# Kernel optimization log

Measured on AMD Instinct MI355X. Metric: run time of the kernel, lower is better.

Reference implementation:

```python
import jax, jax.numpy as jnp
import numpy as np

EMBED_DIM = 2048
NUM_HEADS = 16
HEAD_DIM = EMBED_DIM // NUM_HEADS  # 128
GROUP = 256
NEG = -1e9


def setup_inputs() -> dict:
    key = jax.random.key(0)
    ks = jax.random.split(key, 4)
    B, N, C = 2, 8192, EMBED_DIM
    s = 1.0 / np.sqrt(C).astype(np.float32)
    return {
        "x": jax.random.normal(ks[0], (B, N, C), jnp.float32),
        "Wq": jax.random.normal(ks[1], (C, C), jnp.float32) * s,
        "bq": jnp.zeros((C,), jnp.float32),
        "Wk": jax.random.normal(ks[2], (C, C), jnp.float32) * s,
        "bk": jnp.zeros((C,), jnp.float32),
        "Wv": jax.random.normal(ks[3], (C, C), jnp.float32) * s,
        "bv": jnp.zeros((C,), jnp.float32),
    }


def _s2_attn(x, Wq, bq, Wk, bk, Wv, bv):
    B, N, C = x.shape
    H, hd, gs = NUM_HEADS, HEAD_DIM, GROUP
    G = N // gs
    half = H // 2

    def heads(t):  # [B,N,C] -> [B,H,N,hd]
        return t.reshape(B, N, H, hd).transpose(0, 2, 1, 3)

    q = heads(x @ Wq.T + bq)
    k = heads(x @ Wk.T + bk)
    v = heads(x @ Wv.T + bv)

    def shift(t, s):  # shift second half of heads along sequence
        return jnp.concatenate([t[:, :half], jnp.roll(t[:, half:], s, axis=2)], axis=1)

    q, k, v = shift(q, -(gs // 2)), shift(k, -(gs // 2)), shift(v, -(gs // 2))

    # group-local attention: [B,H,G,gs,hd]
    qg = q.reshape(B, H, G, gs, hd)
    kg = k.reshape(B, H, G, gs, hd)
    vg = v.reshape(B, H, G, gs, hd)

    scores = jnp.einsum("bhgqd,bhgkd->bhgqk", qg, kg) / np.sqrt(hd).astype(x.dtype)
    causal = jnp.triu(jnp.ones((gs, gs), bool), 1)  # mask strictly-upper triangle
    scores = jnp.where(causal, NEG, scores)
    attn = jax.nn.softmax(scores, axis=-1)
    out = jnp.einsum("bhgqk,bhgkd->bhgqd", attn, vg).reshape(B, H, N, hd)

    out = shift(out, gs // 2)  # un-shift the shifted heads
    return out.transpose(0, 2, 1, 3).reshape(B, N, C)


def reference(x, Wq, bq, Wk, bk, Wv, bv):
    return _s2_attn(x, Wq, bq, Wk, bk, Wv, bv)
```

## Files before the change

### kernel.cpp

```cpp
#include <hip/hip_runtime.h>
#include <hip/hip_bf16.h>

#define NSEQ 8192
#define CDIM 2048
#define NHEAD 16
#define HD 128

typedef short short8 __attribute__((ext_vector_type(8)));
typedef short short4v __attribute__((ext_vector_type(4)));
typedef float float4v __attribute__((ext_vector_type(4)));

__device__ __forceinline__ short f2bf(float f) {
    __hip_bfloat16 h = __float2bfloat16(f);
    return *reinterpret_cast<short*>(&h);
}

__device__ __forceinline__ void async_load16(const short* g, short* l) {
    __builtin_amdgcn_global_load_lds((const __attribute__((address_space(1))) void*)g,
                                     (__attribute__((address_space(3))) void*)l,
                                     16, 0, 0);
}

#define X8 (33554432 / 8)
#define W8 (4194304 / 8)

__global__ __launch_bounds__(256) void cvt_all(
    const float* __restrict__ x, const float* __restrict__ wq,
    const float* __restrict__ wk, const float* __restrict__ wv,
    short* __restrict__ xb, short* __restrict__ wqb,
    short* __restrict__ wkb, short* __restrict__ wvb)
{
    const size_t i = (size_t)blockIdx.x * blockDim.x + threadIdx.x;
    const float* src;
    short* dst;
    size_t off;
    if (i < X8)              { src = x;  dst = xb;  off = i; }
    else if (i < X8 + W8)    { src = wq; dst = wqb; off = i - X8; }
    else if (i < X8 + 2*W8)  { src = wk; dst = wkb; off = i - X8 - W8; }
    else                     { src = wv; dst = wvb; off = i - X8 - 2*(size_t)W8; }
    const float4v a = ((const float4v*)src)[off * 2];
    const float4v b = ((const float4v*)src)[off * 2 + 1];
    short8 o;
    for (int j = 0; j < 4; j++) { o[j] = f2bf(a[j]); o[4 + j] = f2bf(b[j]); }
    ((short8*)dst)[off] = o;
}

__global__ __launch_bounds__(256, 2) void qkv_gemm(
    const short* __restrict__ x,
    const short* __restrict__ Wq, const float* __restrict__ bq,
    const short* __restrict__ Wk, const float* __restrict__ bk,
    const short* __restrict__ Wv, const float* __restrict__ bv,
    float* __restrict__ qout, short* __restrict__ kt, short* __restrict__ vt)
{
    __shared__ short As[128 * 32];
    __shared__ short Bs[128 * 32];

    const int tid  = threadIdx.x;
    const int wave = tid >> 6;
    const int lane = tid & 63;
    const int quad = lane >> 4;
    const int l15  = lane & 15;
    const int wm   = wave >> 1;
    const int wn   = wave & 1;

    const int m0  = blockIdx.x * 128;
    const int mat = blockIdx.y >> 4;
    const int h   = blockIdx.y & 15;
    const int n0  = h * HD;

    const short* W    = (mat == 0) ? Wq : (mat == 1) ? Wk : Wv;
    const float* bias = (mat == 0) ? bq : (mat == 1) ? bk : bv;

    const int srow = lane >> 2;
    const int scol = (lane & 3) * 8;

    const float4v fzero = {0.f, 0.f, 0.f, 0.f};
    float4v acc[4][4];
    for (int i = 0; i < 4; i++)
        for (int j = 0; j < 4; j++)
            acc[i][j] = fzero;

    for (int k0 = 0; k0 < CDIM; k0 += 32) {
        __syncthreads();
        for (int c = 0; c < 2; c++) {
            const int chunk = wave * 2 + c;
            const int row   = chunk * 16 + srow;
            async_load16(x + (size_t)(m0 + row) * CDIM + k0 + scol, &As[chunk * 512]);
            async_load16(W + (size_t)(n0 + row) * CDIM + k0 + scol, &Bs[chunk * 512]);
        }
        __syncthreads();

        short8 af[4], bf[4];
        for (int i = 0; i < 4; i++)
            af[i] = *(const short8*)&As[(wm * 64 + i * 16 + l15) * 32 + quad * 8];
        for (int j = 0; j < 4; j++)
            bf[j] = *(const short8*)&Bs[(wn * 64 + j * 16 + l15) * 32 + quad * 8];
        for (int i = 0; i < 4; i++)
            for (int j = 0; j < 4; j++)
                acc[i][j] = __builtin_amdgcn_mfma_f32_16x16x32_bf16(af[i], bf[j],
                                                                    acc[i][j], 0, 0, 0);
    }

    float bvals[4];
    for (int j = 0; j < 4; j++)
        bvals[j] = bias[n0 + wn * 64 + j * 16 + l15];

    for (int i = 0; i < 4; i++) {
        for (int j = 0; j < 4; j++) {
            const int d = wn * 64 + j * 16 + l15;
            for (int r = 0; r < 4; r++) {
                const int m   = m0 + wm * 64 + i * 16 + quad * 4 + r;
                const int b   = m >> 13;
                const int seq = m & (NSEQ - 1);
                const float v = acc[i][j][r] + bvals[j];
                if (mat == 0) {
                    qout[((size_t)(b * NSEQ + seq) << 11) + n0 + d] = v;
                } else {
                    short* outp = (mat == 1) ? kt : vt;
                    outp[(((size_t)(b * NHEAD + h) * NSEQ + seq) << 7) + d] = f2bf(v);
                }
            }
        }
    }
}

__global__ __launch_bounds__(512, 2) void s2_attn(const float* qsrc,
                                                  const short* __restrict__ kt,
                                                  const short* __restrict__ vt,
                                                  float* out)
{
    __shared__ short Ks[64 * 136];
    __shared__ short Vs[64 * 132];
    __shared__ short Ps[8][32 * 40];

    const int bx = blockIdx.x;
    const int g  = bx & 31;
    const int h  = (bx >> 5) & 15;
    const int b  = bx >> 9;
    const int shift = (h >= 8) ? 128 : 0;
    const int sbase = g * 256 + shift;

    const int tid  = threadIdx.x;
    const int wave = tid >> 6;
    const int lane = tid & 63;
    const int quad = lane >> 4;
    const int l15  = lane & 15;

    const size_t bh = ((size_t)b * NHEAD + h) * NSEQ;
    const short* kg = kt + bh * HD;
    const short* vg = vt + bh * HD;

    const int mt0 = wave * 2;

    short8 qf[2][4];
    for (int im = 0; im < 2; im++) {
        const int row = (mt0 + im) * 16 + l15;
        const int p   = (sbase + row) & (NSEQ - 1);
        const float* qr = qsrc + (((size_t)(b * NSEQ + p)) << 11) + h * HD;
        for (int ks = 0; ks < 4; ks++) {
            const float4v qa = *(const float4v*)(qr + ks * 32 + quad * 8);
            const float4v qb = *(const float4v*)(qr + ks * 32 + quad * 8 + 4);
            short8 f;
            for (int j = 0; j < 4; j++) { f[j] = f2bf(qa[j]); f[4 + j] = f2bf(qb[j]); }
            qf[im][ks] = f;
        }
    }

    const float4v fzero = {0.f, 0.f, 0.f, 0.f};
    float4v o[2][8];
    for (int im = 0; im < 2; im++)
        for (int dt = 0; dt < 8; dt++)
            o[im][dt] = fzero;
    float rs[2][4] = {{0.f, 0.f, 0.f, 0.f}, {0.f, 0.f, 0.f, 0.f}};

    for (int kc = 0; kc < 4; kc++) {
        __syncthreads();
        for (int c = 0; c < 2; c++) {
            const int id   = tid + c * 512;
            const int row  = id >> 4;
            const int colb = (id & 15) * 8;
            const int p    = (sbase + kc * 64 + row) & (NSEQ - 1);
            *(short8*)&Ks[row * 136 + colb] = *(const short8*)(kg + (size_t)p * HD + colb);
        }
        for (int c = 0; c < 4; c++) {
            const int id   = tid + c * 512;
            const int row  = id >> 5;
            const int colb = (id & 31) * 4;
            const int p    = (sbase + kc * 64 + row) & (NSEQ - 1);
            *(short4v*)&Vs[row * 132 + colb] = *(const short4v*)(vg + (size_t)p * HD + colb);
        }
        __syncthreads();

        float4v s[2][4];
        for (int im = 0; im < 2; im++)
            for (int nn = 0; nn < 4; nn++)
                s[im][nn] = fzero;
        for (int nn = 0; nn < 4; nn++) {
            short8 kf[4];
            for (int ks = 0; ks < 4; ks++)
                kf[ks] = *(const short8*)&Ks[(nn * 16 + l15) * 136 + ks * 32 + quad * 8];
            for (int im = 0; im < 2; im++)
                for (int ks = 0; ks < 4; ks++)
                    s[im][nn] = __builtin_amdgcn_mfma_f32_16x16x32_bf16(
                        qf[im][ks], kf[ks], s[im][nn], 0, 0, 0);
        }

        for (int half = 0; half < 2; half++) {
            for (int im = 0; im < 2; im++) {
                const int qpos = (mt0 + im) * 16 + quad * 4;
                for (int nn2 = 0; nn2 < 2; nn2++) {
                    const int nn   = half * 2 + nn2;
                    const int kpos = kc * 64 + nn * 16 + l15;
                    for (int r = 0; r < 4; r++) {
                        const float sv = s[im][nn][r] * 0.088388347648318447f;
                        const float pv = (kpos > qpos + r)
                                             ? 0.f
                                             : __expf(fminf(sv, 30.f));
                        rs[im][r] += pv;
                        Ps[wave][(im * 16 + quad * 4 + r) * 40 + nn2 * 16 + l15] = f2bf(pv);
                    }
                }
            }
            __syncthreads();
            short8 pf[2];
            for (int im = 0; im < 2; im++)
                pf[im] = *(const short8*)&Ps[wave][(im * 16 + l15) * 40 + quad * 8];
            for (int dt = 0; dt < 8; dt++) {
                short8 vf;
                for (int jj = 0; jj < 8; jj++)
                    vf[jj] = Vs[(half * 32 + quad * 8 + jj) * 132 + dt * 16 + l15];
                for (int im = 0; im < 2; im++)
                    o[im][dt] = __builtin_amdgcn_mfma_f32_16x16x32_bf16(
                        pf[im], vf, o[im][dt], 0, 0, 0);
            }
            __syncthreads();
        }
    }

    for (int im = 0; im < 2; im++)
        for (int r = 0; r < 4; r++) {
            float v = rs[im][r];
            v += __shfl_xor(v, 1);
            v += __shfl_xor(v, 2);
            v += __shfl_xor(v, 4);
            v += __shfl_xor(v, 8);
            rs[im][r] = v;
        }

    for (int im = 0; im < 2; im++) {
        for (int r = 0; r < 4; r++) {
            const int row = (mt0 + im) * 16 + quad * 4 + r;
            const int p   = (sbase + row) & (NSEQ - 1);
            const float inv = 1.f / rs[im][r];
            const size_t obase = (((size_t)(b * NSEQ + p)) << 11) + h * HD;
            for (int dt = 0; dt < 8; dt++)
                out[obase + dt * 16 + l15] = o[im][dt][r] * inv;
        }
    }
}

extern "C" void kernel_launch(void* const* d_in, const int* in_sizes, int n_in,
                              void* d_out, int out_size, void* d_ws, size_t ws_size,
                              hipStream_t stream) {
    (void)in_sizes; (void)n_in; (void)out_size; (void)ws_size;
    const float* x  = (const float*)d_in[0];
    const float* Wq = (const float*)d_in[1];
    const float* bq = (const float*)d_in[2];
    const float* Wk = (const float*)d_in[3];
    const float* bk = (const float*)d_in[4];
    const float* Wv = (const float*)d_in[5];
    const float* bv = (const float*)d_in[6];

    short* xb  = (short*)d_ws;
    short* wqb = xb  + (size_t)33554432;
    short* wkb = wqb + (size_t)4194304;
    short* wvb = wkb + (size_t)4194304;
    short* kt  = wvb + (size_t)4194304;
    short* vt  = kt  + (size_t)33554432;

    float* outp = (float*)d_out;

    cvt_all<<<dim3(22528), 256, 0, stream>>>(x, Wq, Wk, Wv, xb, wqb, wkb, wvb);
    qkv_gemm<<<dim3(128, 48), 256, 0, stream>>>(xb, wqb, bq, wkb, bk, wvb, bv,
                                                outp, kt, vt);
    s2_attn<<<dim3(1024), 512, 0, stream>>>(outp, kt, vt, outp);
}
```

Before: 874.7 us.

## Skip fully-masked causal tiles, balance waves, and store V transposed with swizzled LDS

Each wave now takes one low and one high query tile (wave and 15-wave) so the causal work is balanced, and both the QK and PV MFMAs are skipped for 64-key chunks that lie entirely above the diagonal. The projection kernel writes V transposed (head dim major, sequence minor), so the attention kernel loads it with 16-byte vector loads into an XOR-swizzled LDS tile and reads V fragments as single short8 loads instead of eight scalar gathers. The per-wave Ps barriers are removed because each wave only touches its own Ps slice. The K and V tile loads drop the per-row wraparound mask and assume a 64-row chunk never crosses the sequence end. The changed V layout also changes the write pattern of the projection kernel, which now scatters with a large stride.

New measurement: 887.2 us. Within noise of the previous version (+1.4%).

```diff
diff --git a/kernel.cpp b/kernel.cpp
--- a/kernel.cpp
+++ b/kernel.cpp
@@ -115,9 +115,10 @@
                 const float v = acc[i][j][r] + bvals[j];
                 if (mat == 0) {
                     qout[((size_t)(b * NSEQ + seq) << 11) + n0 + d] = v;
+                } else if (mat == 1) {
+                    kt[(((size_t)(b * NHEAD + h) * NSEQ + seq) << 7) + d] = f2bf(v);
                 } else {
-                    short* outp = (mat == 1) ? kt : vt;
-                    outp[(((size_t)(b * NHEAD + h) * NSEQ + seq) << 7) + d] = f2bf(v);
+                    vt[(((size_t)(b * NHEAD + h) * HD + d) << 13) + seq] = f2bf(v);
                 }
             }
         }
@@ -130,7 +131,7 @@
                                                   float* out)
 {
     __shared__ short Ks[64 * 136];
-    __shared__ short Vs[64 * 132];
+    __shared__ short VsT[128 * 64];
     __shared__ short Ps[8][32 * 40];
 
     const int bx = blockIdx.x;
@@ -150,11 +151,12 @@
     const short* kg = kt + bh * HD;
     const short* vg = vt + bh * HD;
 
-    const int mt0 = wave * 2;
+    const int mts[2] = { wave, 15 - wave };
+    const int lvl[2] = { wave >> 2, 3 - (wave >> 2) };
 
     short8 qf[2][4];
     for (int im = 0; im < 2; im++) {
-        const int row = (mt0 + im) * 16 + l15;
+        const int row = mts[im] * 16 + l15;
         const int p   = (sbase + row) & (NSEQ - 1);
         const float* qr = qsrc + (((size_t)(b * NSEQ + p)) << 11) + h * HD;
         for (int ks = 0; ks < 4; ks++) {
@@ -174,66 +176,79 @@
     float rs[2][4] = {{0.f, 0.f, 0.f, 0.f}, {0.f, 0.f, 0.f, 0.f}};
 
     for (int kc = 0; kc < 4; kc++) {
+        const int kstart = (sbase + kc * 64) & (NSEQ - 1);
+
         __syncthreads();
-        for (int c = 0; c < 2; c++) {
-            const int id   = tid + c * 512;
-            const int row  = id >> 4;
-            const int colb = (id & 15) * 8;
-            const int p    = (sbase + kc * 64 + row) & (NSEQ - 1);
-            *(short8*)&Ks[row * 136 + colb] = *(const short8*)(kg + (size_t)p * HD + colb);
-        }
-        for (int c = 0; c < 4; c++) {
-            const int id   = tid + c * 512;
-            const int row  = id >> 5;
-            const int colb = (id & 31) * 4;
-            const int p    = (sbase + kc * 64 + row) & (NSEQ - 1);
-            *(short4v*)&Vs[row * 132 + colb] = *(const short4v*)(vg + (size_t)p * HD + colb);
+        {
+            const int row  = tid >> 4;
+            const int colb = (tid & 15) * 8;
+            const short* src = kg + (size_t)(kstart + row) * HD + colb;
+            *(short8*)&Ks[row * 136 + colb] = *(const short8*)src;
+            const int row2 = row + 32;
+            const short* src2 = kg + (size_t)(kstart + row2) * HD + colb;
+            *(short8*)&Ks[row2 * 136 + colb] = *(const short8*)src2;
+        }
+        {
+            const int d0 = tid >> 3;
+            const int gg = tid & 7;
+            *(short8*)&VsT[(d0 * 8 + (gg ^ (d0 & 7))) * 8] =
+                *(const short8*)(vg + (size_t)d0 * NSEQ + kstart + gg * 8);
+            const int d1 = d0 + 64;
+            *(short8*)&VsT[(d1 * 8 + (gg ^ (d1 & 7))) * 8] =
+                *(const short8*)(vg + (size_t)d1 * NSEQ + kstart + gg * 8);
         }
         __syncthreads();
 
+        const bool need0 = (lvl[0] >= kc);
+        const bool need1 = (lvl[1] >= kc);
+        if (!need0 && !need1) continue;
+
         float4v s[2][4];
-        for (int im = 0; im < 2; im++)
-            for (int nn = 0; nn < 4; nn++)
-                s[im][nn] = fzero;
         for (int nn = 0; nn < 4; nn++) {
             short8 kf[4];
             for (int ks = 0; ks < 4; ks++)
                 kf[ks] = *(const short8*)&Ks[(nn * 16 + l15) * 136 + ks * 32 + quad * 8];
-            for (int im = 0; im < 2; im++)
+            for (int im = 0; im < 2; im++) {
+                if (lvl[im] < kc) continue;
+                float4v acc = (nn == 0, fzero), t = fzero;
+                t = s[im][nn] = fzero;
+                (void)acc; (void)t;
                 for (int ks = 0; ks < 4; ks++)
                     s[im][nn] = __builtin_amdgcn_mfma_f32_16x16x32_bf16(
                         qf[im][ks], kf[ks], s[im][nn], 0, 0, 0);
+            }
         }
 
         for (int half = 0; half < 2; half++) {
             for (int im = 0; im < 2; im++) {
-                const int qpos = (mt0 + im) * 16 + quad * 4;
+                if (lvl[im] < kc) continue;
+                const bool diag = (lvl[im] == kc);
+                const int qpos  = (mts[im] & 3) * 16 + quad * 4;
                 for (int nn2 = 0; nn2 < 2; nn2++) {
                     const int nn   = half * 2 + nn2;
-                    const int kpos = kc * 64 + nn * 16 + l15;
+                    const int kpos = nn * 16 + l15;
                     for (int r = 0; r < 4; r++) {
                         const float sv = s[im][nn][r] * 0.088388347648318447f;
-                        const float pv = (kpos > qpos + r)
-                                             ? 0.f
-                                             : __expf(fminf(sv, 30.f));
+                        float pv = __expf(fminf(sv, 30.f));
+                        if (diag && (kpos > qpos + r)) pv = 0.f;
                         rs[im][r] += pv;
                         Ps[wave][(im * 16 + quad * 4 + r) * 40 + nn2 * 16 + l15] = f2bf(pv);
                     }
                 }
             }
-            __syncthreads();
             short8 pf[2];
             for (int im = 0; im < 2; im++)
-                pf[im] = *(const short8*)&Ps[wave][(im * 16 + l15) * 40 + quad * 8];
+                if (lvl[im] >= kc)
+                    pf[im] = *(const short8*)&Ps[wave][(im * 16 + l15) * 40 + quad * 8];
             for (int dt = 0; dt < 8; dt++) {
-                short8 vf;
-                for (int jj = 0; jj < 8; jj++)
-                    vf[jj] = Vs[(half * 32 + quad * 8 + jj) * 132 + dt * 16 + l15];
+                const int dv = dt * 16 + l15;
+                const int gg = (half * 4 + quad) ^ (dv & 7);
+                const short8 vf = *(const short8*)&VsT[(dv * 8 + gg) * 8];
                 for (int im = 0; im < 2; im++)
-                    o[im][dt] = __builtin_amdgcn_mfma_f32_16x16x32_bf16(
-                        pf[im], vf, o[im][dt], 0, 0, 0);
+                    if (lvl[im] >= kc)
+                        o[im][dt] = __builtin_amdgcn_mfma_f32_16x16x32_bf16(
+                            pf[im], vf, o[im][dt], 0, 0, 0);
             }
-            __syncthreads();
         }
     }
 
@@ -249,7 +264,7 @@
 
     for (int im = 0; im < 2; im++) {
         for (int r = 0; r < 4; r++) {
-            const int row = (mt0 + im) * 16 + quad * 4 + r;
+            const int row = mts[im] * 16 + quad * 4 + r;
             const int p   = (sbase + row) & (NSEQ - 1);
             const float inv = 1.f / rs[im][r];
             const size_t obase = (((size_t)(b * NSEQ + p)) << 11) + h * HD;
```
